# Optimization experiments

Measured on AMD Instinct MI355X. Metric: run time of the kernel, lower is better.

The kernel has to match this reference:

```python
import jax, jax.numpy as jnp
import numpy as np

N = 4096
IN_F = 512
OUT_F = 256
HEADS = 4
HEAD_DIM = OUT_F // HEADS


def setup_inputs() -> dict:
    key = jax.random.key(0)
    k_feat, k_adj, k_w, k_a = jax.random.split(key, 4)
    features = jax.random.normal(k_feat, (N, IN_F), dtype=jnp.float32)
    adj_matrix = jax.random.uniform(k_adj, (N, N), dtype=jnp.float32)
    # xavier-uniform-ish init scaled small
    W = jax.random.normal(k_w, (OUT_F, IN_F), dtype=jnp.float32) * (1.0 / np.sqrt(IN_F))
    a = jax.random.normal(k_a, (HEADS, 2 * HEAD_DIM), dtype=jnp.float32) * 0.1
    bias = jnp.zeros((OUT_F,), dtype=jnp.float32)
    return {"features": features, "adj_matrix": adj_matrix, "W": W, "a": a, "bias": bias}


def reference(features, adj_matrix, W, a, bias):
    n = features.shape[0]
    h = features @ W.T                      # [N, OUT_F]
    hh = h.reshape(n, HEADS, HEAD_DIM)      # [N, H, D]
    # e[i,j,h] = leaky_relu(<h_i, a[:, :D]> + <h_j, a[:, D:]>) -- additive decomposition
    e_src = jnp.einsum('nhd,hd->nh', hh, a[:, :HEAD_DIM])   # [N, H]
    e_dst = jnp.einsum('nhd,hd->nh', hh, a[:, HEAD_DIM:])   # [N, H]
    e = e_src[:, None, :] + e_dst[None, :, :]               # [N, N, H]
    e = jnp.where(e >= 0, e, 0.2 * e)                       # leaky_relu(0.2)
    mask = adj_matrix[:, :, None] > 0.1                     # [N, N, 1]
    e = jnp.where(mask, e, -jnp.inf)
    attention = jax.nn.softmax(e, axis=1)                   # softmax over j
    attention = jnp.nan_to_num(attention, nan=0.0)          # fully-masked rows -> 0
    attention_mean = attention.mean(axis=2)                 # [N, N]
    h_out = attention_mean @ h + bias                       # [N, OUT_F]
    return h_out
```

## Files before the change

kernel.cpp:

```cpp
#include <hip/hip_runtime.h>
#include <math.h>

#define NN      4096
#define INF_    512
#define OUTF    256
#define NHEAD   4
#define HDIM    64
#define KSPLIT  8

typedef __attribute__((ext_vector_type(8))) short  short8x;
typedef __attribute__((ext_vector_type(4))) float  float4x;

__device__ __forceinline__ unsigned short f2bf(float x) {
    union { float f; unsigned int u; } c; c.f = x;
    unsigned int r = (c.u + 0x7FFFu + ((c.u >> 16) & 1u)) >> 16;
    return (unsigned short)r;
}
__device__ __forceinline__ float bflo(unsigned int u) {
    union { unsigned int x; float f; } c; c.x = u << 16; return c.f;
}
__device__ __forceinline__ float bfhi(unsigned int u) {
    union { unsigned int x; float f; } c; c.x = u & 0xFFFF0000u; return c.f;
}

__global__ __launch_bounds__(256) void k_prep(const float* __restrict__ feat,
                                              const float* __restrict__ W,
                                              const float* __restrict__ a,
                                              unsigned short* __restrict__ featb,
                                              unsigned short* __restrict__ Wb,
                                              float* __restrict__ wsrc,
                                              float* __restrict__ wdst) {
    const int b = blockIdx.x;
    if (b < 8) {
        const int kk = threadIdx.x & 63, h = threadIdx.x >> 6;
        const int k = b * 64 + kk;
        float s = 0.f, d2 = 0.f;
        #pragma unroll 8
        for (int d = 0; d < 64; ++d) {
            float wv = W[(size_t)(h * HDIM + d) * INF_ + k];
            s  += wv * a[h * 2 * HDIM + d];
            d2 += wv * a[h * 2 * HDIM + HDIM + d];
        }
        wsrc[k * NHEAD + h] = s;
        wdst[k * NHEAD + h] = d2;
        return;
    }
    const int bb = b - 8;
    const float* src;
    unsigned short* dst;
    int idx;
    if (bb < 2048) { src = feat; dst = featb; idx = bb * 1024 + threadIdx.x * 4; }
    else           { src = W;    dst = Wb;    idx = (bb - 2048) * 1024 + threadIdx.x * 4; }
    float4x v = *(const float4x*)(src + idx);
    ushort4 u;
    u.x = f2bf(v[0]); u.y = f2bf(v[1]); u.z = f2bf(v[2]); u.w = f2bf(v[3]);
    *(ushort4*)(dst + idx) = u;
}

__global__ __launch_bounds__(256) void k_edge(const float* __restrict__ feat,
                                              const float* __restrict__ wsrc,
                                              const float* __restrict__ wdst,
                                              float* __restrict__ es,
                                              unsigned short* __restrict__ Bt,
                                              unsigned short* __restrict__ Dt) {
    const int r = blockIdx.x * 16 + (threadIdx.x >> 4);
    const int lane = threadIdx.x & 15;
    float s[4] = {0.f, 0.f, 0.f, 0.f};
    float d[4] = {0.f, 0.f, 0.f, 0.f};
    for (int kk = 0; kk < 32; ++kk) {
        int k = kk * 16 + lane;
        float f = feat[(size_t)r * INF_ + k];
        float4x ws = ((const float4x*)wsrc)[k];
        float4x wd = ((const float4x*)wdst)[k];
        #pragma unroll
        for (int h = 0; h < 4; ++h) { s[h] += f * ws[h]; d[h] += f * wd[h]; }
    }
    #pragma unroll
    for (int off = 1; off < 16; off <<= 1) {
        #pragma unroll
        for (int h = 0; h < 4; ++h) {
            s[h] += __shfl_xor(s[h], off);
            d[h] += __shfl_xor(d[h], off);
        }
    }
    if (lane == 0) {
        #pragma unroll
        for (int h = 0; h < 4; ++h) {
            es[r * NHEAD + h] = s[h];
            Bt[r * NHEAD + h] = f2bf(__expf(d[h]));
            Dt[r * NHEAD + h] = f2bf(__expf(0.2f * d[h]));
        }
    }
}

__global__ __launch_bounds__(256) void k_h_gemm(const unsigned short* __restrict__ featb,
                                                const unsigned short* __restrict__ Wb,
                                                unsigned short* __restrict__ hT) {
    __shared__ __align__(16) unsigned short lds_f[64 * 40];
    __shared__ __align__(16) unsigned short lds_w[64 * 40];
    const int tid  = threadIdx.x;
    const int w    = tid >> 6;
    const int lane = tid & 63;
    const int lidx = lane & 15;
    const int quad = lane >> 4;
    const int o0 = blockIdx.x * 64;
    const int i0 = blockIdx.y * 64;
    const int sr = tid >> 2;
    const int skq = (tid & 3) * 8;

    float4x acc[4];
    #pragma unroll
    for (int nt = 0; nt < 4; ++nt) acc[nt] = (float4x){0.f, 0.f, 0.f, 0.f};

    ushort4 pf0 = *(const ushort4*)&featb[(size_t)(i0 + sr) * INF_ + skq];
    ushort4 pf1 = *(const ushort4*)&featb[(size_t)(i0 + sr) * INF_ + skq + 4];
    ushort4 pw0 = *(const ushort4*)&Wb[(size_t)(o0 + sr) * INF_ + skq];
    ushort4 pw1 = *(const ushort4*)&Wb[(size_t)(o0 + sr) * INF_ + skq + 4];

    for (int kt = 0; kt < INF_; kt += 32) {
        __syncthreads();
        *(ushort4*)&lds_f[sr * 40 + skq]     = pf0;
        *(ushort4*)&lds_f[sr * 40 + skq + 4] = pf1;
        *(ushort4*)&lds_w[sr * 40 + skq]     = pw0;
        *(ushort4*)&lds_w[sr * 40 + skq + 4] = pw1;
        __syncthreads();
        if (kt + 32 < INF_) {
            int kn = kt + 32;
            pf0 = *(const ushort4*)&featb[(size_t)(i0 + sr) * INF_ + kn + skq];
            pf1 = *(const ushort4*)&featb[(size_t)(i0 + sr) * INF_ + kn + skq + 4];
            pw0 = *(const ushort4*)&Wb[(size_t)(o0 + sr) * INF_ + kn + skq];
            pw1 = *(const ushort4*)&Wb[(size_t)(o0 + sr) * INF_ + kn + skq + 4];
        }
        short8x af = *(const short8x*)&lds_f[(w * 16 + lidx) * 40 + quad * 8];
        short8x bw[4];
        #pragma unroll
        for (int t = 0; t < 4; ++t)
            bw[t] = *(const short8x*)&lds_w[(t * 16 + lidx) * 40 + quad * 8];
        #pragma unroll
        for (int nt = 0; nt < 4; ++nt)
            acc[nt] = __builtin_amdgcn_mfma_f32_16x16x32_bf16(af, bw[nt], acc[nt], 0, 0, 0);
    }
    #pragma unroll
    for (int nt = 0; nt < 4; ++nt) {
        int col = o0 + nt * 16 + lidx;
        int m0r = i0 + w * 16 + quad * 4;
        ushort4 u;
        u.x = f2bf(acc[nt][0]); u.y = f2bf(acc[nt][1]);
        u.z = f2bf(acc[nt][2]); u.w = f2bf(acc[nt][3]);
        *(ushort4*)&hT[(size_t)col * NN + m0r] = u;
    }
}

__global__ __launch_bounds__(256) void k_attn(const float* __restrict__ adj,
                                              const float* __restrict__ es,
                                              const unsigned short* __restrict__ Bt,
                                              const unsigned short* __restrict__ Dt,
                                              unsigned short* __restrict__ attn) {
    __shared__ float red[2][2][8];
    __shared__ float cfs[2][8];
    const int tid = threadIdx.x;
    const int r  = tid >> 7;
    const int l  = tid & 127;
    const int wv = (tid >> 6) & 1;
    const int i  = blockIdx.x * 2 + r;

    const float4x esv = ((const float4x*)es)[i];
    float TB[4];
    #pragma unroll
    for (int h = 0; h < 4; ++h) TB[h] = __expf(-esv[h]);
    const float4x* arow4 = (const float4x*)(adj + (size_t)i * NN);
    const uint4* B4 = (const uint4*)Bt;
    const uint4* D4 = (const uint4*)Dt;

    float S1[4] = {0.f, 0.f, 0.f, 0.f};
    float S2[4] = {0.f, 0.f, 0.f, 0.f};
    #pragma unroll
    for (int it = 0; it < 8; ++it) {
        int jv = it * 128 + l;
        float4x av = arow4[jv];
        uint4 bu0 = B4[jv * 2], bu1 = B4[jv * 2 + 1];
        uint4 du0 = D4[jv * 2], du1 = D4[jv * 2 + 1];
        unsigned int bwv[8] = {bu0.x, bu0.y, bu0.z, bu0.w, bu1.x, bu1.y, bu1.z, bu1.w};
        unsigned int dwv[8] = {du0.x, du0.y, du0.z, du0.w, du1.x, du1.y, du1.z, du1.w};
        #pragma unroll
        for (int u = 0; u < 4; ++u) {
            bool m = av[u] > 0.1f;
            float b0 = bflo(bwv[u * 2]), b1 = bfhi(bwv[u * 2]);
            float b2 = bflo(bwv[u * 2 + 1]), b3 = bfhi(bwv[u * 2 + 1]);
            float d0 = bflo(dwv[u * 2]), d1 = bfhi(dwv[u * 2]);
            float d2 = bflo(dwv[u * 2 + 1]), d3 = bfhi(dwv[u * 2 + 1]);
            bool p0 = b0 >= TB[0], p1 = b1 >= TB[1], p2 = b2 >= TB[2], p3 = b3 >= TB[3];
            S1[0] += (m && p0) ? b0 : 0.f;   S2[0] += (m && !p0) ? d0 : 0.f;
            S1[1] += (m && p1) ? b1 : 0.f;   S2[1] += (m && !p1) ? d1 : 0.f;
            S1[2] += (m && p2) ? b2 : 0.f;   S2[2] += (m && !p2) ? d2 : 0.f;
            S1[3] += (m && p3) ? b3 : 0.f;   S2[3] += (m && !p3) ? d3 : 0.f;
        }
    }
    #pragma unroll
    for (int off = 1; off < 64; off <<= 1) {
        #pragma unroll
        for (int h = 0; h < 4; ++h) {
            S1[h] += __shfl_xor(S1[h], off);
            S2[h] += __shfl_xor(S2[h], off);
        }
    }
    if ((tid & 63) == 0) {
        #pragma unroll
        for (int h = 0; h < 4; ++h) { red[r][wv][h] = S1[h]; red[r][wv][4 + h] = S2[h]; }
    }
    __syncthreads();
    if (tid < 8) {
        int rr = tid >> 2, h = tid & 3;
        int ii = blockIdx.x * 2 + rr;
        float s1 = red[rr][0][h] + red[rr][1][h];
        float s2 = red[rr][0][4 + h] + red[rr][1][4 + h];
        float e = es[ii * NHEAD + h];
        float A = __expf(e), C = __expf(0.2f * e);
        float den = A * s1 + C * s2;
        float sc = den > 0.f ? 0.25f / den : 0.f;
        cfs[rr][h]     = A * sc;
        cfs[rr][4 + h] = C * sc;
    }
    __syncthreads();
    float cA[4], cC[4];
    #pragma unroll
    for (int h = 0; h < 4; ++h) { cA[h] = cfs[r][h]; cC[h] = cfs[r][4 + h]; }

    unsigned short* orow = attn + (size_t)i * NN;
    #pragma unroll
    for (int it = 0; it < 8; ++it) {
        int jv = it * 128 + l;
        float4x av = arow4[jv];
        uint4 bu0 = B4[jv * 2], bu1 = B4[jv * 2 + 1];
        uint4 du0 = D4[jv * 2], du1 = D4[jv * 2 + 1];
        unsigned int bwv[8] = {bu0.x, bu0.y, bu0.z, bu0.w, bu1.x, bu1.y, bu1.z, bu1.w};
        unsigned int dwv[8] = {du0.x, du0.y, du0.z, du0.w, du1.x, du1.y, du1.z, du1.w};
        ushort4 o;
        unsigned short* op = (unsigned short*)&o;
        #pragma unroll
        for (int u = 0; u < 4; ++u) {
            float b0 = bflo(bwv[u * 2]), b1 = bfhi(bwv[u * 2]);
            float b2 = bflo(bwv[u * 2 + 1]), b3 = bfhi(bwv[u * 2 + 1]);
            float d0 = bflo(dwv[u * 2]), d1 = bfhi(dwv[u * 2]);
            float d2 = bflo(dwv[u * 2 + 1]), d3 = bfhi(dwv[u * 2 + 1]);
            float p;
            p  = (b0 >= TB[0]) ? cA[0] * b0 : cC[0] * d0;
            p += (b1 >= TB[1]) ? cA[1] * b1 : cC[1] * d1;
            p += (b2 >= TB[2]) ? cA[2] * b2 : cC[2] * d2;
            p += (b3 >= TB[3]) ? cA[3] * b3 : cC[3] * d3;
            op[u] = f2bf((av[u] > 0.1f) ? p : 0.f);
        }
        *(ushort4*)&orow[jv * 4] = o;
    }
}

__global__ __launch_bounds__(256) void k_out_gemm(const unsigned short* __restrict__ attn,
                                                  const unsigned short* __restrict__ hT,
                                                  float* __restrict__ partials) {
    __shared__ __align__(16) unsigned short lds_a[64 * 40];
    __shared__ __align__(16) unsigned short lds_h[256 * 40];
    const int tid  = threadIdx.x;
    const int w    = tid >> 6;
    const int lane = tid & 63;
    const int lidx = lane & 15;
    const int quad = lane >> 4;
    const int i0    = blockIdx.x * 64;
    const int kbase = blockIdx.y * (NN / KSPLIT);
    const int srow = tid >> 3;
    const int skq  = tid & 7;

    float4x acc[4][4];
    #pragma unroll
    for (int a = 0; a < 4; ++a)
        #pragma unroll
        for (int b = 0; b < 4; ++b)
            acc[a][b] = (float4x){0.f, 0.f, 0.f, 0.f};

    ushort4 pa[2], ph[8];
    #pragma unroll
    for (int it = 0; it < 2; ++it)
        pa[it] = *(const ushort4*)&attn[(size_t)(i0 + it * 32 + srow) * NN + kbase + skq * 4];
    #pragma unroll
    for (int it = 0; it < 8; ++it)
        ph[it] = *(const ushort4*)&hT[(size_t)(it * 32 + srow) * NN + kbase + skq * 4];

    const int KSTEPS = (NN / KSPLIT) / 32;
    for (int ks = 0; ks < KSTEPS; ++ks) {
        __syncthreads();
        #pragma unroll
        for (int it = 0; it < 2; ++it)
            *(ushort4*)&lds_a[(it * 32 + srow) * 40 + skq * 4] = pa[it];
        #pragma unroll
        for (int it = 0; it < 8; ++it)
            *(ushort4*)&lds_h[(it * 32 + srow) * 40 + skq * 4] = ph[it];
        __syncthreads();
        if (ks < KSTEPS - 1) {
            const int ktn = kbase + (ks + 1) * 32;
            #pragma unroll
            for (int it = 0; it < 2; ++it)
                pa[it] = *(const ushort4*)&attn[(size_t)(i0 + it * 32 + srow) * NN + ktn + skq * 4];
            #pragma unroll
            for (int it = 0; it < 8; ++it)
                ph[it] = *(const ushort4*)&hT[(size_t)(it * 32 + srow) * NN + ktn + skq * 4];
        }
        short8x af[4], bfr[4];
        #pragma unroll
        for (int t = 0; t < 4; ++t) {
            af[t]  = *(const short8x*)&lds_a[(t * 16 + lidx) * 40 + quad * 8];
            bfr[t] = *(const short8x*)&lds_h[(w * 64 + t * 16 + lidx) * 40 + quad * 8];
        }
        #pragma unroll
        for (int it = 0; it < 4; ++it)
            #pragma unroll
            for (int nt = 0; nt < 4; ++nt)
                acc[it][nt] = __builtin_amdgcn_mfma_f32_16x16x32_bf16(
                    af[it], bfr[nt], acc[it][nt], 0, 0, 0);
    }
    float* pbase = partials + (size_t)blockIdx.y * NN * OUTF;
    #pragma unroll
    for (int it = 0; it < 4; ++it)
        #pragma unroll
        for (int nt = 0; nt < 4; ++nt)
            #pragma unroll
            for (int rr = 0; rr < 4; ++rr) {
                int row = i0 + it * 16 + quad * 4 + rr;
                int col = w * 64 + nt * 16 + lidx;
                pbase[(size_t)row * OUTF + col] = acc[it][nt][rr];
            }
}

__global__ __launch_bounds__(256) void k_reduce_out(const float* __restrict__ partials,
                                                    const float* __restrict__ bias,
                                                    float* __restrict__ out) {
    const int i = blockIdx.x;
    const int n = threadIdx.x;
    float acc = bias[n];
    #pragma unroll
    for (int s = 0; s < KSPLIT; ++s)
        acc += partials[((size_t)s * NN + i) * OUTF + n];
    out[(size_t)i * OUTF + n] = acc;
}

extern "C" void kernel_launch(void* const* d_in, const int* in_sizes, int n_in,
                              void* d_out, int out_size, void* d_ws, size_t ws_size,
                              hipStream_t stream) {
    const float* feat = (const float*)d_in[0];
    const float* adj  = (const float*)d_in[1];
    const float* W    = (const float*)d_in[2];
    const float* a    = (const float*)d_in[3];
    const float* bias = (const float*)d_in[4];
    float* out = (float*)d_out;

    char* ws = (char*)d_ws;
    float*          es    = (float*)(ws + 0);
    unsigned short* Btb   = (unsigned short*)(ws + (64u << 10));
    unsigned short* Dtb   = (unsigned short*)(ws + (96u << 10));
    float*          wsrc  = (float*)(ws + (128u << 10));
    float*          wdst  = (float*)(ws + (160u << 10));
    unsigned short* hT    = (unsigned short*)(ws + (256u << 10));
    unsigned short* attn  = (unsigned short*)(ws + (2560u << 10));
    unsigned short* featb = (unsigned short*)(ws + (2560u << 10));
    unsigned short* Wb    = (unsigned short*)(ws + (6656u << 10));
    float*          partials = (float*)(ws + (35328u << 10));

    k_prep      <<<2184,             256, 0, stream>>>(feat, W, a, featb, Wb, wsrc, wdst);
    k_edge      <<<256,              256, 0, stream>>>(feat, wsrc, wdst, es, Btb, Dtb);
    k_h_gemm    <<<dim3(4, 64),      256, 0, stream>>>(featb, Wb, hT);
    k_attn      <<<2048,             256, 0, stream>>>(adj, es, Btb, Dtb, attn);
    k_out_gemm  <<<dim3(64, KSPLIT), 256, 0, stream>>>(attn, hT, partials);
    k_reduce_out<<<NN,               256, 0, stream>>>(partials, bias, out);
}
```

Before: 184.0 us.

## Merge edge and h-GEMM kernels, atomically reduce split-K output, register-cache attention rows

Folds the edge-score kernel into the h-projection GEMM launch as extra blocks, and initializes the output with bias inside the prep kernel. The split-K partials buffer and its reduction kernel are replaced by relaxed atomic adds straight into the output. The attention kernel now handles one row per block and keeps the adjacency and exp tables in registers between the two passes, so it no longer re-reads them. This removes two launches and the partials round-trip through memory, at the cost of atomic contention, non-deterministic summation order, and higher register pressure in the attention kernel.

```diff
diff --git a/kernel.cpp b/kernel.cpp
--- a/kernel.cpp
+++ b/kernel.cpp
@@ -26,10 +26,12 @@
 __global__ __launch_bounds__(256) void k_prep(const float* __restrict__ feat,
                                               const float* __restrict__ W,
                                               const float* __restrict__ a,
+                                              const float* __restrict__ bias,
                                               unsigned short* __restrict__ featb,
                                               unsigned short* __restrict__ Wb,
                                               float* __restrict__ wsrc,
-                                              float* __restrict__ wdst) {
+                                              float* __restrict__ wdst,
+                                              float* __restrict__ out) {
     const int b = blockIdx.x;
     if (b < 8) {
         const int kk = threadIdx.x & 63, h = threadIdx.x >> 6;
@@ -45,6 +47,12 @@
         wdst[k * NHEAD + h] = d2;
         return;
     }
+    if (b >= 2184) {
+        const int idx = (b - 2184) * 1024 + threadIdx.x * 4;
+        float4x bv = *(const float4x*)&bias[idx & 255];
+        *(float4x*)&out[idx] = bv;
+        return;
+    }
     const int bb = b - 8;
     const float* src;
     unsigned short* dst;
@@ -57,54 +65,55 @@
     *(ushort4*)(dst + idx) = u;
 }
 
-__global__ __launch_bounds__(256) void k_edge(const float* __restrict__ feat,
-                                              const float* __restrict__ wsrc,
-                                              const float* __restrict__ wdst,
-                                              float* __restrict__ es,
-                                              unsigned short* __restrict__ Bt,
-                                              unsigned short* __restrict__ Dt) {
-    const int r = blockIdx.x * 16 + (threadIdx.x >> 4);
-    const int lane = threadIdx.x & 15;
-    float s[4] = {0.f, 0.f, 0.f, 0.f};
-    float d[4] = {0.f, 0.f, 0.f, 0.f};
-    for (int kk = 0; kk < 32; ++kk) {
-        int k = kk * 16 + lane;
-        float f = feat[(size_t)r * INF_ + k];
-        float4x ws = ((const float4x*)wsrc)[k];
-        float4x wd = ((const float4x*)wdst)[k];
-        #pragma unroll
-        for (int h = 0; h < 4; ++h) { s[h] += f * ws[h]; d[h] += f * wd[h]; }
-    }
-    #pragma unroll
-    for (int off = 1; off < 16; off <<= 1) {
-        #pragma unroll
-        for (int h = 0; h < 4; ++h) {
-            s[h] += __shfl_xor(s[h], off);
-            d[h] += __shfl_xor(d[h], off);
-        }
-    }
-    if (lane == 0) {
-        #pragma unroll
-        for (int h = 0; h < 4; ++h) {
-            es[r * NHEAD + h] = s[h];
-            Bt[r * NHEAD + h] = f2bf(__expf(d[h]));
-            Dt[r * NHEAD + h] = f2bf(__expf(0.2f * d[h]));
-        }
-    }
-}
-
-__global__ __launch_bounds__(256) void k_h_gemm(const unsigned short* __restrict__ featb,
-                                                const unsigned short* __restrict__ Wb,
-                                                unsigned short* __restrict__ hT) {
+__global__ __launch_bounds__(256) void k_mid(const unsigned short* __restrict__ featb,
+                                             const unsigned short* __restrict__ Wb,
+                                             const float* __restrict__ feat,
+                                             const float* __restrict__ wsrc,
+                                             const float* __restrict__ wdst,
+                                             unsigned short* __restrict__ hT,
+                                             float* __restrict__ es,
+                                             unsigned short* __restrict__ Bt,
+                                             unsigned short* __restrict__ Dt) {
     __shared__ __align__(16) unsigned short lds_f[64 * 40];
     __shared__ __align__(16) unsigned short lds_w[64 * 40];
-    const int tid  = threadIdx.x;
+    const int tid = threadIdx.x;
+    if (blockIdx.x >= 256) {
+        const int r = (blockIdx.x - 256) * 16 + (tid >> 4);
+        const int lane = tid & 15;
+        float s[4] = {0.f, 0.f, 0.f, 0.f};
+        float d[4] = {0.f, 0.f, 0.f, 0.f};
+        for (int kk = 0; kk < 32; ++kk) {
+            int k = kk * 16 + lane;
+            float f = feat[(size_t)r * INF_ + k];
+            float4x wsv = ((const float4x*)wsrc)[k];
+            float4x wdv = ((const float4x*)wdst)[k];
+            #pragma unroll
+            for (int h = 0; h < 4; ++h) { s[h] += f * wsv[h]; d[h] += f * wdv[h]; }
+        }
+        #pragma unroll
+        for (int off = 1; off < 16; off <<= 1) {
+            #pragma unroll
+            for (int h = 0; h < 4; ++h) {
+                s[h] += __shfl_xor(s[h], off);
+                d[h] += __shfl_xor(d[h], off);
+            }
+        }
+        if (lane == 0) {
+            #pragma unroll
+            for (int h = 0; h < 4; ++h) {
+                es[r * NHEAD + h] = s[h];
+                Bt[r * NHEAD + h] = f2bf(__expf(d[h]));
+                Dt[r * NHEAD + h] = f2bf(__expf(0.2f * d[h]));
+            }
+        }
+        return;
+    }
     const int w    = tid >> 6;
     const int lane = tid & 63;
     const int lidx = lane & 15;
     const int quad = lane >> 4;
-    const int o0 = blockIdx.x * 64;
-    const int i0 = blockIdx.y * 64;
+    const int o0 = (blockIdx.x & 3) * 64;
+    const int i0 = (blockIdx.x >> 2) * 64;
     const int sr = tid >> 2;
     const int skq = (tid & 3) * 8;
 
@@ -151,18 +160,17 @@
     }
 }
 
-__global__ __launch_bounds__(256) void k_attn(const float* __restrict__ adj,
-                                              const float* __restrict__ es,
-                                              const unsigned short* __restrict__ Bt,
-                                              const unsigned short* __restrict__ Dt,
-                                              unsigned short* __restrict__ attn) {
-    __shared__ float red[2][2][8];
-    __shared__ float cfs[2][8];
+__global__ __launch_bounds__(256, 4) void k_attn(const float* __restrict__ adj,
+                                                 const float* __restrict__ es,
+                                                 const unsigned short* __restrict__ Bt,
+                                                 const unsigned short* __restrict__ Dt,
+                                                 unsigned short* __restrict__ attn) {
+    __shared__ float red[4][8];
+    __shared__ float cfs[8];
     const int tid = threadIdx.x;
-    const int r  = tid >> 7;
-    const int l  = tid & 127;
-    const int wv = (tid >> 6) & 1;
-    const int i  = blockIdx.x * 2 + r;
+    const int wv  = tid >> 6;
+    const int lane = tid & 63;
+    const int i = blockIdx.x;
 
     const float4x esv = ((const float4x*)es)[i];
     float TB[4];
@@ -172,23 +180,31 @@
     const uint4* B4 = (const uint4*)Bt;
     const uint4* D4 = (const uint4*)Dt;
 
+    float4x av[4];
+    uint4 bu[8], du[8];
+    #pragma unroll
+    for (int t = 0; t < 4; ++t) {
+        int jv = t * 256 + tid;
+        av[t] = arow4[jv];
+        bu[2 * t]     = B4[jv * 2];
+        bu[2 * t + 1] = B4[jv * 2 + 1];
+        du[2 * t]     = D4[jv * 2];
+        du[2 * t + 1] = D4[jv * 2 + 1];
+    }
+
     float S1[4] = {0.f, 0.f, 0.f, 0.f};
     float S2[4] = {0.f, 0.f, 0.f, 0.f};
     #pragma unroll
-    for (int it = 0; it < 8; ++it) {
-        int jv = it * 128 + l;
-        float4x av = arow4[jv];
-        uint4 bu0 = B4[jv * 2], bu1 = B4[jv * 2 + 1];
-        uint4 du0 = D4[jv * 2], du1 = D4[jv * 2 + 1];
-        unsigned int bwv[8] = {bu0.x, bu0.y, bu0.z, bu0.w, bu1.x, bu1.y, bu1.z, bu1.w};
-        unsigned int dwv[8] = {du0.x, du0.y, du0.z, du0.w, du1.x, du1.y, du1.z, du1.w};
+    for (int t = 0; t < 4; ++t) {
+        const unsigned int* bup = (const unsigned int*)&bu[2 * t];
+        const unsigned int* dup = (const unsigned int*)&du[2 * t];
         #pragma unroll
         for (int u = 0; u < 4; ++u) {
-            bool m = av[u] > 0.1f;
-            float b0 = bflo(bwv[u * 2]), b1 = bfhi(bwv[u * 2]);
-            float b2 = bflo(bwv[u * 2 + 1]), b3 = bfhi(bwv[u * 2 + 1]);
-            float d0 = bflo(dwv[u * 2]), d1 = bfhi(dwv[u * 2]);
-            float d2 = bflo(dwv[u * 2 + 1]), d3 = bfhi(dwv[u * 2 + 1]);
+            bool m = av[t][u] > 0.1f;
+            unsigned int bwA = bup[u * 2], bwB = bup[u * 2 + 1];
+            unsigned int dwA = dup[u * 2], dwB = dup[u * 2 + 1];
+            float b0 = bflo(bwA), b1 = bfhi(bwA), b2 = bflo(bwB), b3 = bfhi(bwB);
+            float d0 = bflo(dwA), d1 = bfhi(dwA), d2 = bflo(dwB), d3 = bfhi(dwB);
             bool p0 = b0 >= TB[0], p1 = b1 >= TB[1], p2 = b2 >= TB[2], p3 = b3 >= TB[3];
             S1[0] += (m && p0) ? b0 : 0.f;   S2[0] += (m && !p0) ? d0 : 0.f;
             S1[1] += (m && p1) ? b1 : 0.f;   S2[1] += (m && !p1) ? d1 : 0.f;
@@ -204,59 +220,51 @@
             S2[h] += __shfl_xor(S2[h], off);
         }
     }
-    if ((tid & 63) == 0) {
-        #pragma unroll
-        for (int h = 0; h < 4; ++h) { red[r][wv][h] = S1[h]; red[r][wv][4 + h] = S2[h]; }
+    if (lane == 0) {
+        #pragma unroll
+        for (int h = 0; h < 4; ++h) { red[wv][h] = S1[h]; red[wv][4 + h] = S2[h]; }
     }
     __syncthreads();
-    if (tid < 8) {
-        int rr = tid >> 2, h = tid & 3;
-        int ii = blockIdx.x * 2 + rr;
-        float s1 = red[rr][0][h] + red[rr][1][h];
-        float s2 = red[rr][0][4 + h] + red[rr][1][4 + h];
-        float e = es[ii * NHEAD + h];
-        float A = __expf(e), C = __expf(0.2f * e);
-        float den = A * s1 + C * s2;
-        float sc = den > 0.f ? 0.25f / den : 0.f;
-        cfs[rr][h]     = A * sc;
-        cfs[rr][4 + h] = C * sc;
-    }
+    if (tid < 8)
+        cfs[tid] = red[0][tid] + red[1][tid] + red[2][tid] + red[3][tid];
     __syncthreads();
     float cA[4], cC[4];
     #pragma unroll
-    for (int h = 0; h < 4; ++h) { cA[h] = cfs[r][h]; cC[h] = cfs[r][4 + h]; }
+    for (int h = 0; h < 4; ++h) {
+        float A = __expf(esv[h]), C = __expf(0.2f * esv[h]);
+        float den = A * cfs[h] + C * cfs[4 + h];
+        float sc = den > 0.f ? 0.25f / den : 0.f;
+        cA[h] = A * sc;
+        cC[h] = C * sc;
+    }
 
     unsigned short* orow = attn + (size_t)i * NN;
     #pragma unroll
-    for (int it = 0; it < 8; ++it) {
-        int jv = it * 128 + l;
-        float4x av = arow4[jv];
-        uint4 bu0 = B4[jv * 2], bu1 = B4[jv * 2 + 1];
-        uint4 du0 = D4[jv * 2], du1 = D4[jv * 2 + 1];
-        unsigned int bwv[8] = {bu0.x, bu0.y, bu0.z, bu0.w, bu1.x, bu1.y, bu1.z, bu1.w};
-        unsigned int dwv[8] = {du0.x, du0.y, du0.z, du0.w, du1.x, du1.y, du1.z, du1.w};
+    for (int t = 0; t < 4; ++t) {
+        const unsigned int* bup = (const unsigned int*)&bu[2 * t];
+        const unsigned int* dup = (const unsigned int*)&du[2 * t];
         ushort4 o;
         unsigned short* op = (unsigned short*)&o;
         #pragma unroll
         for (int u = 0; u < 4; ++u) {
-            float b0 = bflo(bwv[u * 2]), b1 = bfhi(bwv[u * 2]);
-            float b2 = bflo(bwv[u * 2 + 1]), b3 = bfhi(bwv[u * 2 + 1]);
-            float d0 = bflo(dwv[u * 2]), d1 = bfhi(dwv[u * 2]);
-            float d2 = bflo(dwv[u * 2 + 1]), d3 = bfhi(dwv[u * 2 + 1]);
+            unsigned int bwA = bup[u * 2], bwB = bup[u * 2 + 1];
+            unsigned int dwA = dup[u * 2], dwB = dup[u * 2 + 1];
+            float b0 = bflo(bwA), b1 = bfhi(bwA), b2 = bflo(bwB), b3 = bfhi(bwB);
+            float d0 = bflo(dwA), d1 = bfhi(dwA), d2 = bflo(dwB), d3 = bfhi(dwB);
             float p;
             p  = (b0 >= TB[0]) ? cA[0] * b0 : cC[0] * d0;
             p += (b1 >= TB[1]) ? cA[1] * b1 : cC[1] * d1;
             p += (b2 >= TB[2]) ? cA[2] * b2 : cC[2] * d2;
             p += (b3 >= TB[3]) ? cA[3] * b3 : cC[3] * d3;
-            op[u] = f2bf((av[u] > 0.1f) ? p : 0.f);
-        }
-        *(ushort4*)&orow[jv * 4] = o;
+            op[u] = f2bf((av[t][u] > 0.1f) ? p : 0.f);
+        }
+        *(ushort4*)&orow[(t * 256 + tid) * 4] = o;
     }
 }
 
 __global__ __launch_bounds__(256) void k_out_gemm(const unsigned short* __restrict__ attn,
                                                   const unsigned short* __restrict__ hT,
-                                                  float* __restrict__ partials) {
+                                                  float* __restrict__ out) {
     __shared__ __align__(16) unsigned short lds_a[64 * 40];
     __shared__ __align__(16) unsigned short lds_h[256 * 40];
     const int tid  = threadIdx.x;
@@ -316,29 +324,18 @@
                 acc[it][nt] = __builtin_amdgcn_mfma_f32_16x16x32_bf16(
                     af[it], bfr[nt], acc[it][nt], 0, 0, 0);
     }
-    float* pbase = partials + (size_t)blockIdx.y * NN * OUTF;
     #pragma unroll
     for (int it = 0; it < 4; ++it)
         #pragma unroll
-        for (int nt = 0; nt < 4; ++nt)
-            #pragma unroll
-            for (int rr = 0; rr < 4; ++rr) {
-                int row = i0 + it * 16 + quad * 4 + rr;
-                int col = w * 64 + nt * 16 + lidx;
-                pbase[(size_t)row * OUTF + col] = acc[it][nt][rr];
-            }
-}
-
-__global__ __launch_bounds__(256) void k_reduce_out(const float* __restrict__ partials,
-                                                    const float* __restrict__ bias,
-                                                    float* __restrict__ out) {
-    const int i = blockIdx.x;
-    const int n = threadIdx.x;
-    float acc = bias[n];
-    #pragma unroll
-    for (int s = 0; s < KSPLIT; ++s)
-        acc += partials[((size_t)s * NN + i) * OUTF + n];
-    out[(size_t)i * OUTF + n] = acc;
+        for (int nt = 0; nt < 4; ++nt) {
+            int col = w * 64 + nt * 16 + lidx;
+            int row0 = i0 + it * 16 + quad * 4;
+            #pragma unroll
+            for (int rr = 0; rr < 4; ++rr)
+                __hip_atomic_fetch_add(&out[(size_t)(row0 + rr) * OUTF + col],
+                                       acc[it][nt][rr],
+                                       __ATOMIC_RELAXED, __HIP_MEMORY_SCOPE_AGENT);
+        }
 }
 
 extern "C" void kernel_launch(void* const* d_in, const int* in_sizes, int n_in,
@@ -361,12 +358,9 @@
     unsigned short* attn  = (unsigned short*)(ws + (2560u << 10));
     unsigned short* featb = (unsigned short*)(ws + (2560u << 10));
     unsigned short* Wb    = (unsigned short*)(ws + (6656u << 10));
-    float*          partials = (float*)(ws + (35328u << 10));
-
-    k_prep      <<<2184,             256, 0, stream>>>(feat, W, a, featb, Wb, wsrc, wdst);
-    k_edge      <<<256,              256, 0, stream>>>(feat, wsrc, wdst, es, Btb, Dtb);
-    k_h_gemm    <<<dim3(4, 64),      256, 0, stream>>>(featb, Wb, hT);
-    k_attn      <<<2048,             256, 0, stream>>>(adj, es, Btb, Dtb, attn);
-    k_out_gemm  <<<dim3(64, KSPLIT), 256, 0, stream>>>(attn, hT, partials);
-    k_reduce_out<<<NN,               256, 0, stream>>>(partials, bias, out);
-}
+
+    k_prep    <<<3208,             256, 0, stream>>>(feat, W, a, bias, featb, Wb, wsrc, wdst, out);
+    k_mid     <<<512,              256, 0, stream>>>(featb, Wb, feat, wsrc, wdst, hT, es, Btb, Dtb);
+    k_attn    <<<NN,               256, 0, stream>>>(adj, es, Btb, Dtb, attn);
+    k_out_gemm<<<dim3(64, KSPLIT), 256, 0, stream>>>(attn, hT, out);
+}
```

Result: slower. 233.5 us (+26.9%).

## Fuse edge-score computation into h GEMM epilogue and give each attention row its own block

Applied to the files above, without the earlier changes.

Removes the separate W·a precompute and edge kernels. The h GEMM now has each block compute a full 64x256 output tile, so the per-head src/dst scores can be reduced from the accumulators in the epilogue. The GEMM drops to 64 blocks and loses its register prefetch double-buffering, which lowers parallelism and latency hiding. The attention kernel switches to one row per block, caches the adjacency values in registers so the second pass does not reload them, and computes the normalisation in every thread, with twice as many blocks as before.

```diff
diff --git a/kernel.cpp b/kernel.cpp
--- a/kernel.cpp
+++ b/kernel.cpp
@@ -23,132 +23,110 @@
     union { unsigned int x; float f; } c; c.x = u & 0xFFFF0000u; return c.f;
 }
 
-__global__ __launch_bounds__(256) void k_prep(const float* __restrict__ feat,
+__global__ __launch_bounds__(256) void k_cast(const float* __restrict__ feat,
                                               const float* __restrict__ W,
-                                              const float* __restrict__ a,
                                               unsigned short* __restrict__ featb,
-                                              unsigned short* __restrict__ Wb,
-                                              float* __restrict__ wsrc,
-                                              float* __restrict__ wdst) {
+                                              unsigned short* __restrict__ Wb) {
     const int b = blockIdx.x;
-    if (b < 8) {
-        const int kk = threadIdx.x & 63, h = threadIdx.x >> 6;
-        const int k = b * 64 + kk;
-        float s = 0.f, d2 = 0.f;
-        #pragma unroll 8
-        for (int d = 0; d < 64; ++d) {
-            float wv = W[(size_t)(h * HDIM + d) * INF_ + k];
-            s  += wv * a[h * 2 * HDIM + d];
-            d2 += wv * a[h * 2 * HDIM + HDIM + d];
-        }
-        wsrc[k * NHEAD + h] = s;
-        wdst[k * NHEAD + h] = d2;
-        return;
-    }
-    const int bb = b - 8;
     const float* src;
     unsigned short* dst;
     int idx;
-    if (bb < 2048) { src = feat; dst = featb; idx = bb * 1024 + threadIdx.x * 4; }
-    else           { src = W;    dst = Wb;    idx = (bb - 2048) * 1024 + threadIdx.x * 4; }
+    if (b < 2048) { src = feat; dst = featb; idx = b * 1024 + threadIdx.x * 4; }
+    else          { src = W;    dst = Wb;    idx = (b - 2048) * 1024 + threadIdx.x * 4; }
     float4x v = *(const float4x*)(src + idx);
     ushort4 u;
     u.x = f2bf(v[0]); u.y = f2bf(v[1]); u.z = f2bf(v[2]); u.w = f2bf(v[3]);
     *(ushort4*)(dst + idx) = u;
 }
 
-__global__ __launch_bounds__(256) void k_edge(const float* __restrict__ feat,
-                                              const float* __restrict__ wsrc,
-                                              const float* __restrict__ wdst,
-                                              float* __restrict__ es,
-                                              unsigned short* __restrict__ Bt,
-                                              unsigned short* __restrict__ Dt) {
-    const int r = blockIdx.x * 16 + (threadIdx.x >> 4);
-    const int lane = threadIdx.x & 15;
-    float s[4] = {0.f, 0.f, 0.f, 0.f};
-    float d[4] = {0.f, 0.f, 0.f, 0.f};
-    for (int kk = 0; kk < 32; ++kk) {
-        int k = kk * 16 + lane;
-        float f = feat[(size_t)r * INF_ + k];
-        float4x ws = ((const float4x*)wsrc)[k];
-        float4x wd = ((const float4x*)wdst)[k];
-        #pragma unroll
-        for (int h = 0; h < 4; ++h) { s[h] += f * ws[h]; d[h] += f * wd[h]; }
-    }
-    #pragma unroll
-    for (int off = 1; off < 16; off <<= 1) {
-        #pragma unroll
-        for (int h = 0; h < 4; ++h) {
-            s[h] += __shfl_xor(s[h], off);
-            d[h] += __shfl_xor(d[h], off);
-        }
-    }
-    if (lane == 0) {
-        #pragma unroll
-        for (int h = 0; h < 4; ++h) {
-            es[r * NHEAD + h] = s[h];
-            Bt[r * NHEAD + h] = f2bf(__expf(d[h]));
-            Dt[r * NHEAD + h] = f2bf(__expf(0.2f * d[h]));
-        }
-    }
-}
-
-__global__ __launch_bounds__(256) void k_h_gemm(const unsigned short* __restrict__ featb,
-                                                const unsigned short* __restrict__ Wb,
-                                                unsigned short* __restrict__ hT) {
+__global__ __launch_bounds__(256) void k_hedge(const unsigned short* __restrict__ featb,
+                                               const unsigned short* __restrict__ Wb,
+                                               const float* __restrict__ a,
+                                               unsigned short* __restrict__ hT,
+                                               float* __restrict__ es,
+                                               unsigned short* __restrict__ Bt,
+                                               unsigned short* __restrict__ Dt) {
     __shared__ __align__(16) unsigned short lds_f[64 * 40];
-    __shared__ __align__(16) unsigned short lds_w[64 * 40];
+    __shared__ __align__(16) unsigned short lds_w[256 * 40];
     const int tid  = threadIdx.x;
     const int w    = tid >> 6;
     const int lane = tid & 63;
     const int lidx = lane & 15;
     const int quad = lane >> 4;
-    const int o0 = blockIdx.x * 64;
-    const int i0 = blockIdx.y * 64;
+    const int i0   = blockIdx.x * 64;
     const int sr = tid >> 2;
     const int skq = (tid & 3) * 8;
 
-    float4x acc[4];
-    #pragma unroll
-    for (int nt = 0; nt < 4; ++nt) acc[nt] = (float4x){0.f, 0.f, 0.f, 0.f};
-
-    ushort4 pf0 = *(const ushort4*)&featb[(size_t)(i0 + sr) * INF_ + skq];
-    ushort4 pf1 = *(const ushort4*)&featb[(size_t)(i0 + sr) * INF_ + skq + 4];
-    ushort4 pw0 = *(const ushort4*)&Wb[(size_t)(o0 + sr) * INF_ + skq];
-    ushort4 pw1 = *(const ushort4*)&Wb[(size_t)(o0 + sr) * INF_ + skq + 4];
+    float4x acc[4][4];
+    #pragma unroll
+    for (int p = 0; p < 4; ++p)
+        #pragma unroll
+        for (int q = 0; q < 4; ++q)
+            acc[p][q] = (float4x){0.f, 0.f, 0.f, 0.f};
 
     for (int kt = 0; kt < INF_; kt += 32) {
         __syncthreads();
-        *(ushort4*)&lds_f[sr * 40 + skq]     = pf0;
-        *(ushort4*)&lds_f[sr * 40 + skq + 4] = pf1;
-        *(ushort4*)&lds_w[sr * 40 + skq]     = pw0;
-        *(ushort4*)&lds_w[sr * 40 + skq + 4] = pw1;
+        *(ushort4*)&lds_f[sr * 40 + skq]     = *(const ushort4*)&featb[(size_t)(i0 + sr) * INF_ + kt + skq];
+        *(ushort4*)&lds_f[sr * 40 + skq + 4] = *(const ushort4*)&featb[(size_t)(i0 + sr) * INF_ + kt + skq + 4];
+        #pragma unroll
+        for (int itr = 0; itr < 4; ++itr) {
+            int n = itr * 64 + sr;
+            *(ushort4*)&lds_w[n * 40 + skq]     = *(const ushort4*)&Wb[(size_t)n * INF_ + kt + skq];
+            *(ushort4*)&lds_w[n * 40 + skq + 4] = *(const ushort4*)&Wb[(size_t)n * INF_ + kt + skq + 4];
+        }
         __syncthreads();
-        if (kt + 32 < INF_) {
-            int kn = kt + 32;
-            pf0 = *(const ushort4*)&featb[(size_t)(i0 + sr) * INF_ + kn + skq];
-            pf1 = *(const ushort4*)&featb[(size_t)(i0 + sr) * INF_ + kn + skq + 4];
-            pw0 = *(const ushort4*)&Wb[(size_t)(o0 + sr) * INF_ + kn + skq];
-            pw1 = *(const ushort4*)&Wb[(size_t)(o0 + sr) * INF_ + kn + skq + 4];
-        }
-        short8x af = *(const short8x*)&lds_f[(w * 16 + lidx) * 40 + quad * 8];
-        short8x bw[4];
-        #pragma unroll
-        for (int t = 0; t < 4; ++t)
-            bw[t] = *(const short8x*)&lds_w[(t * 16 + lidx) * 40 + quad * 8];
-        #pragma unroll
-        for (int nt = 0; nt < 4; ++nt)
-            acc[nt] = __builtin_amdgcn_mfma_f32_16x16x32_bf16(af, bw[nt], acc[nt], 0, 0, 0);
-    }
+        short8x af[4], bw[4];
+        #pragma unroll
+        for (int t = 0; t < 4; ++t) {
+            af[t] = *(const short8x*)&lds_f[(t * 16 + lidx) * 40 + quad * 8];
+            bw[t] = *(const short8x*)&lds_w[(w * 64 + t * 16 + lidx) * 40 + quad * 8];
+        }
+        #pragma unroll
+        for (int it = 0; it < 4; ++it)
+            #pragma unroll
+            for (int nt = 0; nt < 4; ++nt)
+                acc[it][nt] = __builtin_amdgcn_mfma_f32_16x16x32_bf16(
+                    af[it], bw[nt], acc[it][nt], 0, 0, 0);
+    }
+    #pragma unroll
+    for (int it = 0; it < 4; ++it)
+        #pragma unroll
+        for (int nt = 0; nt < 4; ++nt) {
+            int col = w * 64 + nt * 16 + lidx;
+            int m0r = i0 + it * 16 + quad * 4;
+            ushort4 u;
+            u.x = f2bf(acc[it][nt][0]); u.y = f2bf(acc[it][nt][1]);
+            u.z = f2bf(acc[it][nt][2]); u.w = f2bf(acc[it][nt][3]);
+            *(ushort4*)&hT[(size_t)col * NN + m0r] = u;
+        }
+    float asrc[4], adst[4];
     #pragma unroll
     for (int nt = 0; nt < 4; ++nt) {
-        int col = o0 + nt * 16 + lidx;
-        int m0r = i0 + w * 16 + quad * 4;
-        ushort4 u;
-        u.x = f2bf(acc[nt][0]); u.y = f2bf(acc[nt][1]);
-        u.z = f2bf(acc[nt][2]); u.w = f2bf(acc[nt][3]);
-        *(ushort4*)&hT[(size_t)col * NN + m0r] = u;
-    }
+        asrc[nt] = a[w * 2 * HDIM + nt * 16 + lidx];
+        adst[nt] = a[w * 2 * HDIM + HDIM + nt * 16 + lidx];
+    }
+    #pragma unroll
+    for (int it = 0; it < 4; ++it)
+        #pragma unroll
+        for (int r = 0; r < 4; ++r) {
+            float s = 0.f, d = 0.f;
+            #pragma unroll
+            for (int nt = 0; nt < 4; ++nt) {
+                s += acc[it][nt][r] * asrc[nt];
+                d += acc[it][nt][r] * adst[nt];
+            }
+            #pragma unroll
+            for (int off = 1; off < 16; off <<= 1) {
+                s += __shfl_xor(s, off);
+                d += __shfl_xor(d, off);
+            }
+            if (lidx == 0) {
+                int row = i0 + it * 16 + quad * 4 + r;
+                es[row * NHEAD + w] = s;
+                Bt[row * NHEAD + w] = f2bf(__expf(d));
+                Dt[row * NHEAD + w] = f2bf(__expf(0.2f * d));
+            }
+        }
 }
 
 __global__ __launch_bounds__(256) void k_attn(const float* __restrict__ adj,
@@ -156,13 +134,12 @@
                                               const unsigned short* __restrict__ Bt,
                                               const unsigned short* __restrict__ Dt,
                                               unsigned short* __restrict__ attn) {
-    __shared__ float red[2][2][8];
-    __shared__ float cfs[2][8];
+    __shared__ float red[4][8];
+    __shared__ float cfs[8];
     const int tid = threadIdx.x;
-    const int r  = tid >> 7;
-    const int l  = tid & 127;
-    const int wv = (tid >> 6) & 1;
-    const int i  = blockIdx.x * 2 + r;
+    const int wv  = tid >> 6;
+    const int lane = tid & 63;
+    const int i = blockIdx.x;
 
     const float4x esv = ((const float4x*)es)[i];
     float TB[4];
@@ -172,19 +149,20 @@
     const uint4* B4 = (const uint4*)Bt;
     const uint4* D4 = (const uint4*)Dt;
 
+    float4x av[4];
     float S1[4] = {0.f, 0.f, 0.f, 0.f};
     float S2[4] = {0.f, 0.f, 0.f, 0.f};
     #pragma unroll
-    for (int it = 0; it < 8; ++it) {
-        int jv = it * 128 + l;
-        float4x av = arow4[jv];
+    for (int t = 0; t < 4; ++t) {
+        int jv = t * 256 + tid;
+        av[t] = arow4[jv];
         uint4 bu0 = B4[jv * 2], bu1 = B4[jv * 2 + 1];
         uint4 du0 = D4[jv * 2], du1 = D4[jv * 2 + 1];
         unsigned int bwv[8] = {bu0.x, bu0.y, bu0.z, bu0.w, bu1.x, bu1.y, bu1.z, bu1.w};
         unsigned int dwv[8] = {du0.x, du0.y, du0.z, du0.w, du1.x, du1.y, du1.z, du1.w};
         #pragma unroll
         for (int u = 0; u < 4; ++u) {
-            bool m = av[u] > 0.1f;
+            bool m = av[t][u] > 0.1f;
             float b0 = bflo(bwv[u * 2]), b1 = bfhi(bwv[u * 2]);
             float b2 = bflo(bwv[u * 2 + 1]), b3 = bfhi(bwv[u * 2 + 1]);
             float d0 = bflo(dwv[u * 2]), d1 = bfhi(dwv[u * 2]);
@@ -204,33 +182,28 @@
             S2[h] += __shfl_xor(S2[h], off);
         }
     }
-    if ((tid & 63) == 0) {
-        #pragma unroll
-        for (int h = 0; h < 4; ++h) { red[r][wv][h] = S1[h]; red[r][wv][4 + h] = S2[h]; }
+    if (lane == 0) {
+        #pragma unroll
+        for (int h = 0; h < 4; ++h) { red[wv][h] = S1[h]; red[wv][4 + h] = S2[h]; }
     }
     __syncthreads();
-    if (tid < 8) {
-        int rr = tid >> 2, h = tid & 3;
-        int ii = blockIdx.x * 2 + rr;
-        float s1 = red[rr][0][h] + red[rr][1][h];
-        float s2 = red[rr][0][4 + h] + red[rr][1][4 + h];
-        float e = es[ii * NHEAD + h];
-        float A = __expf(e), C = __expf(0.2f * e);
-        float den = A * s1 + C * s2;
-        float sc = den > 0.f ? 0.25f / den : 0.f;
-        cfs[rr][h]     = A * sc;
-        cfs[rr][4 + h] = C * sc;
-    }
+    if (tid < 8)
+        cfs[tid] = red[0][tid] + red[1][tid] + red[2][tid] + red[3][tid];
     __syncthreads();
     float cA[4], cC[4];
     #pragma unroll
-    for (int h = 0; h < 4; ++h) { cA[h] = cfs[r][h]; cC[h] = cfs[r][4 + h]; }
+    for (int h = 0; h < 4; ++h) {
+        float A = __expf(esv[h]), C = __expf(0.2f * esv[h]);
+        float den = A * cfs[h] + C * cfs[4 + h];
+        float sc = den > 0.f ? 0.25f / den : 0.f;
+        cA[h] = A * sc;
+        cC[h] = C * sc;
+    }
 
     unsigned short* orow = attn + (size_t)i * NN;
     #pragma unroll
-    for (int it = 0; it < 8; ++it) {
-        int jv = it * 128 + l;
-        float4x av = arow4[jv];
+    for (int t = 0; t < 4; ++t) {
+        int jv = t * 256 + tid;
         uint4 bu0 = B4[jv * 2], bu1 = B4[jv * 2 + 1];
         uint4 du0 = D4[jv * 2], du1 = D4[jv * 2 + 1];
         unsigned int bwv[8] = {bu0.x, bu0.y, bu0.z, bu0.w, bu1.x, bu1.y, bu1.z, bu1.w};
@@ -248,7 +221,7 @@
             p += (b1 >= TB[1]) ? cA[1] * b1 : cC[1] * d1;
             p += (b2 >= TB[2]) ? cA[2] * b2 : cC[2] * d2;
             p += (b3 >= TB[3]) ? cA[3] * b3 : cC[3] * d3;
-            op[u] = f2bf((av[u] > 0.1f) ? p : 0.f);
+            op[u] = f2bf((av[t][u] > 0.1f) ? p : 0.f);
         }
         *(ushort4*)&orow[jv * 4] = o;
     }
@@ -271,10 +244,10 @@
 
     float4x acc[4][4];
     #pragma unroll
-    for (int a = 0; a < 4; ++a)
-        #pragma unroll
-        for (int b = 0; b < 4; ++b)
-            acc[a][b] = (float4x){0.f, 0.f, 0.f, 0.f};
+    for (int p = 0; p < 4; ++p)
+        #pragma unroll
+        for (int q = 0; q < 4; ++q)
+            acc[p][q] = (float4x){0.f, 0.f, 0.f, 0.f};
 
     ushort4 pa[2], ph[8];
     #pragma unroll
@@ -355,18 +328,15 @@
     float*          es    = (float*)(ws + 0);
     unsigned short* Btb   = (unsigned short*)(ws + (64u << 10));
     unsigned short* Dtb   = (unsigned short*)(ws + (96u << 10));
-    float*          wsrc  = (float*)(ws + (128u << 10));
-    float*          wdst  = (float*)(ws + (160u << 10));
     unsigned short* hT    = (unsigned short*)(ws + (256u << 10));
     unsigned short* attn  = (unsigned short*)(ws + (2560u << 10));
     unsigned short* featb = (unsigned short*)(ws + (2560u << 10));
     unsigned short* Wb    = (unsigned short*)(ws + (6656u << 10));
     float*          partials = (float*)(ws + (35328u << 10));
 
-    k_prep      <<<2184,             256, 0, stream>>>(feat, W, a, featb, Wb, wsrc, wdst);
-    k_edge      <<<256,              256, 0, stream>>>(feat, wsrc, wdst, es, Btb, Dtb);
-    k_h_gemm    <<<dim3(4, 64),      256, 0, stream>>>(featb, Wb, hT);
-    k_attn      <<<2048,             256, 0, stream>>>(adj, es, Btb, Dtb, attn);
+    k_cast      <<<2176,             256, 0, stream>>>(feat, W, featb, Wb);
+    k_hedge     <<<64,               256, 0, stream>>>(featb, Wb, a, hT, es, Btb, Dtb);
+    k_attn      <<<NN,               256, 0, stream>>>(adj, es, Btb, Dtb, attn);
     k_out_gemm  <<<dim3(64, KSPLIT), 256, 0, stream>>>(attn, hT, partials);
     k_reduce_out<<<NN,               256, 0, stream>>>(partials, bias, out);
 }
```

Measured after the change: 183.8 us. Within noise of the previous version (-0.1%).
